# Kernel tuning notes

Measured on AMD Instinct MI355X. Metric: run time of the kernel, lower is better.

## Reference

```python
import jax, jax.numpy as jnp
import numpy as np

BITS = 4
N_PACK = 8          # 32-bit words / 4-bit values
GROUPSIZE = 128
MASK = (1 << BITS) - 1


def dequantize(qweight, qzeros, scales):
    """GPTQ/optimum-format int4 dequant.
    qweight: [in/8, out] int32, little-endian nibbles along packed (input) dim.
    qzeros:  [groups, out/8] int32, little-endian nibbles along packed (output) dim.
    scales:  [groups, out] float.
    Returns W: [in, out] float.
    """
    shifts = (jnp.arange(N_PACK, dtype=jnp.int32) * BITS)
    kpack, out_f = qweight.shape
    groups = scales.shape[0]
    # unpack weight nibbles -> [in, out]
    w_int = (qweight[:, None, :] >> shifts[None, :, None]) & MASK        # [in/8, 8, out]
    w_int = w_int.reshape(kpack * N_PACK, out_f)                          # [in, out]
    # unpack zero-point nibbles -> [groups, out]; optimum format adds 1 back
    zp = (qzeros[:, :, None] >> shifts[None, None, :]) & MASK             # [groups, out/8, 8]
    zp = zp.reshape(groups, out_f) + 1                                    # [groups, out]
    # group-wise dequant: (w - zp) * scale
    w_g = w_int.reshape(groups, GROUPSIZE, out_f).astype(scales.dtype)    # [G, gs, out]
    W = (w_g - zp[:, None, :].astype(scales.dtype)) * scales[:, None, :]
    return W.reshape(kpack * N_PACK, out_f)


def setup_inputs() -> dict:
    key = jax.random.key(0)
    k1, k2, k3, k4, k5 = jax.random.split(key, 5)
    in_f, out_f, groups = 4096, 11008, 4096 // GROUPSIZE
    tokens = 4096
    x = jax.random.normal(k1, (tokens, in_f), dtype=jnp.float32)
    qweight = jax.random.randint(k2, (in_f // N_PACK, out_f), 0, 2147483647, dtype=jnp.int32)
    qzeros = jax.random.randint(k3, (groups, out_f // N_PACK), 0, 2147483647, dtype=jnp.int32)
    scales = jax.random.uniform(k4, (groups, out_f), dtype=jnp.float32) * 0.01 + 0.001
    bias = jax.random.normal(k5, (out_f,), dtype=jnp.float32)
    return {"x": x, "qweight": qweight, "qzeros": qzeros, "scales": scales, "bias": bias}


def reference(x, qweight, qzeros, scales, bias):
    W = dequantize(qweight, qzeros, scales)   # [in, out]
    return x @ W + bias                        # F.linear(x, W.T, bias)
```

## Files before the change

### kernel.cpp

```cpp
#include <hip/hip_runtime.h>
#include <stdint.h>

typedef _Float16 h2 __attribute__((ext_vector_type(2)));
typedef _Float16 h8 __attribute__((ext_vector_type(8)));
typedef float f32x4 __attribute__((ext_vector_type(4)));

__device__ __forceinline__ uint32_t pk_cvt(float a, float b) {
  return __builtin_bit_cast(uint32_t, __builtin_amdgcn_cvt_pkrtz(a, b));
}

__device__ __forceinline__ uint32_t dq(uint32_t t, h2 z2, h2 s2) {
  h2 v = __builtin_bit_cast(h2, t);
  h2 w = (v - z2) * s2;
  return __builtin_bit_cast(uint32_t, w);
}

__device__ __forceinline__ uint32_t dq_lin(uint32_t u, h2 z2, h2 s2) {
  uint32_t t = (u & 0xFu) | ((u & 0xF0u) << 12) | 0x64006400u;
  return dq(t, z2, s2);
}

typedef __attribute__((address_space(1))) const uint32_t* gas_ptr;
typedef __attribute__((address_space(3))) uint32_t* las_ptr;
__device__ __forceinline__ void gll16(const _Float16* g, _Float16* l) {
  __builtin_amdgcn_global_load_lds((gas_ptr)g, (las_ptr)l, 16, 0, 0);
}

#define WAITVM(n) asm volatile("s_waitcnt vmcnt(" #n ")" ::: "memory")
#define WAITLGKM(n) asm volatile("s_waitcnt lgkmcnt(" #n ")" ::: "memory")
#define MEMFENCE  asm volatile("" ::: "memory")
#define SB __builtin_amdgcn_sched_barrier(0)

__global__ __launch_bounds__(256) void cvt_x_kernel(const float* __restrict__ x,
                                                    _Float16* __restrict__ xh,
                                                    size_t n) {
  size_t i = ((size_t)blockIdx.x * 256 + threadIdx.x) * 8;
  if (i >= n) return;
  float4 a = *(const float4*)(x + i);
  float4 b = *(const float4*)(x + i + 4);
  uint4 v = make_uint4(pk_cvt(a.x, a.y), pk_cvt(a.z, a.w),
                       pk_cvt(b.x, b.y), pk_cvt(b.z, b.w));
  *(uint4*)(xh + i) = v;
}

__global__ __launch_bounds__(512, 2) void gemm_f16_fusedB(
    const _Float16* __restrict__ A, const uint32_t* __restrict__ qweight,
    const uint32_t* __restrict__ qzeros, const float* __restrict__ scales,
    const float* __restrict__ bias, float* __restrict__ out,
    int M, int N, int K) {
  __shared__ _Float16 As[4][256 * 32];
  __shared__ _Float16 Bs[4][256 * 32];

  const int gx = gridDim.x, gy = gridDim.y;
  const int nwg = gx * gy;
  const int lin = blockIdx.y * gx + blockIdx.x;
  const int xcd = lin & 7, idx = lin >> 3;
  const int q8 = nwg >> 3, r8 = nwg & 7;
  const int wg = (xcd < r8 ? xcd * (q8 + 1) : r8 * (q8 + 1) + (xcd - r8) * q8) + idx;
  const int bn0 = (wg % gx) * 256;
  const int bm0 = (wg / gx) * 256;

  const int tid = threadIdx.x;
  const int lane = tid & 63;
  const int wave = tid >> 6;
  const int wm = wave >> 2;
  const int wn = wave & 3;

  f32x4 acc[8][4];
#pragma unroll
  for (int i = 0; i < 8; ++i)
#pragma unroll
    for (int j = 0; j < 4; ++j) acc[i][j] = (f32x4)0.f;

  const int srow = lane >> 2;
  const int sslot = (lane & 3) ^ ((lane >> 3) & 3);
  const _Float16* pSa0 = A + (size_t)(bm0 + 32 * wave + srow) * K + sslot * 8;
  const _Float16* pSa1 = pSa0 + (size_t)16 * K;
  const int dst_off = wave * 1024;

  const int bcol = tid & 255;
  const int kpo = tid >> 8;
  const int ncol = bn0 + bcol;
  const int NP = N >> 3;
  const uint32_t* qbase = qweight + ncol;
  const uint32_t* qzbase = qzeros + (ncol >> 3);
  const float* scbase = scales + ncol;
  const int bw0 = bcol * 32 + ((kpo)     ^ ((bcol >> 1) & 3)) * 8;
  const int bw1 = bcol * 32 + ((kpo + 2) ^ ((bcol >> 1) & 3)) * 8;

  const int fslot = ((lane >> 4) ^ ((lane >> 1) & 3)) * 8;
  const int aoff = (wm * 128 + (lane & 15)) * 32 + fslot;
  const int boff = (wn * 64 + (lane & 15)) * 32 + fslot;

  const int nt = K >> 5;

  uint32_t qE0 = 0, qE1 = 0, qzE = 0; float scE = 0.f;
  uint32_t qO0 = 0, qO1 = 0, qzO = 0; float scO = 0.f;

#define GLLA(u) {                                                         \
    const size_t ko_ = (size_t)(u) * 32;                                  \
    _Float16* da_ = &As[(u) & 3][0] + dst_off;                            \
    gll16(pSa0 + ko_, da_);                                               \
    gll16(pSa1 + ko_, da_ + 512);                                         \
  }

#define QLOAD(SET, u) {                                                   \
    const size_t kpb_ = (size_t)(u) * 4 + kpo;                            \
    q##SET##0 = qbase[kpb_ * N];                                          \
    q##SET##1 = qbase[(kpb_ + 2) * N];                                    \
    const int g_ = (u) >> 2;                                              \
    qz##SET = qzbase[(size_t)g_ * NP];                                    \
    sc##SET = scbase[(size_t)g_ * N];                                     \
  }

#define DEQW(SET, u) {                                                    \
    int zp_ = (qz##SET >> ((ncol & 7) * 4)) & 15;                         \
    _Float16 hz_ = (_Float16)(float)(1024 + zp_ + 1);                     \
    _Float16 hs_ = (_Float16)sc##SET;                                     \
    h2 z2_ = {hz_, hz_}, s2_ = {hs_, hs_};                                \
    _Float16* bb_ = &Bs[(u) & 3][0];                                      \
    uint4 v0_ = make_uint4(dq_lin(q##SET##0, z2_, s2_),                   \
                           dq_lin(q##SET##0 >> 8, z2_, s2_),              \
                           dq_lin(q##SET##0 >> 16, z2_, s2_),             \
                           dq_lin(q##SET##0 >> 24, z2_, s2_));            \
    uint4 v1_ = make_uint4(dq_lin(q##SET##1, z2_, s2_),                   \
                           dq_lin(q##SET##1 >> 8, z2_, s2_),              \
                           dq_lin(q##SET##1 >> 16, z2_, s2_),             \
                           dq_lin(q##SET##1 >> 24, z2_, s2_));            \
    *(uint4*)(bb_ + bw0) = v0_;                                           \
    *(uint4*)(bb_ + bw1) = v1_;                                           \
  }

#define ITER_BODY(T, CS, LS)                                              \
  {                                                                       \
    __builtin_amdgcn_s_barrier();                                         \
    MEMFENCE;                                                             \
    const int buf_ = (T) & 3;                                             \
    const _Float16* Ab_ = &As[buf_][0] + aoff;                            \
    const _Float16* Bb_ = &Bs[buf_][0] + boff;                            \
    h8 bf_[4], af0_[4], af1_[4];                                          \
    _Pragma("unroll") for (int r = 0; r < 4; ++r)                         \
        bf_[r] = *(const h8*)(Bb_ + r * 512);                             \
    _Pragma("unroll") for (int r = 0; r < 4; ++r)                         \
        af0_[r] = *(const h8*)(Ab_ + r * 512);                            \
    _Pragma("unroll") for (int r = 0; r < 4; ++r)                         \
        af1_[r] = *(const h8*)(Ab_ + (4 + r) * 512);                      \
    SB;                                                                   \
    if ((T) + 2 < nt) QLOAD(LS, (T) + 2);                                 \
    SB;                                                                   \
    if ((T) + 3 < nt) GLLA((T) + 3);                                      \
    SB;                                                                   \
    if ((T) + 1 < nt) {                                                   \
      if ((T) + 4 <= nt) { WAITVM(8); }                                   \
      else if ((T) + 3 == nt) { WAITVM(6); }                              \
      else { WAITVM(0); }                                                 \
      SB;                                                                 \
      DEQW(CS, (T) + 1);                                                  \
      WAITLGKM(6);                                                        \
    } else {                                                              \
      WAITLGKM(4);                                                        \
    }                                                                     \
    SB;                                                                   \
    __builtin_amdgcn_s_setprio(1);                                        \
    _Pragma("unroll") for (int r = 0; r < 4; ++r)                         \
      _Pragma("unroll") for (int j = 0; j < 4; ++j)                       \
        acc[r][j] = __builtin_amdgcn_mfma_f32_16x16x32_f16(               \
            af0_[r], bf_[j], acc[r][j], 0, 0, 0);                         \
    __builtin_amdgcn_s_setprio(0);                                        \
    WAITLGKM(0);                                                          \
    SB;                                                                   \
    __builtin_amdgcn_s_setprio(1);                                        \
    _Pragma("unroll") for (int r = 0; r < 4; ++r)                         \
      _Pragma("unroll") for (int j = 0; j < 4; ++j)                       \
        acc[4 + r][j] = __builtin_amdgcn_mfma_f32_16x16x32_f16(           \
            af1_[r], bf_[j], acc[4 + r][j], 0, 0, 0);                     \
    __builtin_amdgcn_s_setprio(0);                                        \
  }

  GLLA(0); SB;
  QLOAD(E, 0); SB;
  GLLA(1); SB;
  QLOAD(O, 1); SB;
  GLLA(2); SB;
  WAITVM(8);
  SB;
  DEQW(E, 0);
  WAITLGKM(0);

  for (int t = 0; t < nt; t += 2) {
    ITER_BODY(t, O, E);
    ITER_BODY(t + 1, E, O);
  }

  const int r0 = bm0 + wm * 128 + ((lane >> 4) << 2);
  const int c0 = bn0 + wn * 64 + (lane & 15);
#pragma unroll
  for (int j = 0; j < 4; ++j) {
    const int c = c0 + j * 16;
    const float bv = bias[c];
#pragma unroll
    for (int i = 0; i < 8; ++i) {
#pragma unroll
      for (int rr = 0; rr < 4; ++rr)
        out[(size_t)(r0 + i * 16 + rr) * N + c] = acc[i][j][rr] + bv;
    }
  }
#undef GLLA
#undef QLOAD
#undef DEQW
#undef ITER_BODY
}

#define LDK 40
__global__ __launch_bounds__(256) void gptq_gemm_fused(
    const float* __restrict__ x, const uint32_t* __restrict__ qweight,
    const uint32_t* __restrict__ qzeros, const float* __restrict__ scales,
    const float* __restrict__ bias, float* __restrict__ out,
    int M, int N, int K) {
  __shared__ _Float16 As[128 * LDK];
  __shared__ _Float16 Bs[128 * LDK];
  const int tid = threadIdx.x, lane = tid & 63, wave = tid >> 6;
  const int wm = wave & 1, wn = wave >> 1;
  const int bn0 = blockIdx.x * 128, bm0 = blockIdx.y * 128;
  const int sr = tid >> 1, sg0 = (tid & 1) * 2;
  const float* xrow = x + (size_t)(bm0 + sr) * K + sg0 * 8;
  const int colb = bn0 + sr;
  const int groups = K >> 7, NP = N >> 3;
  f32x4 acc[4][4];
#pragma unroll
  for (int i = 0; i < 4; ++i)
#pragma unroll
    for (int j = 0; j < 4; ++j) acc[i][j] = (f32x4)0.f;
  const _Float16* Ab = As + (wm * 64 + (lane & 15)) * LDK + (lane >> 4) * 8;
  const _Float16* Bb = Bs + (wn * 64 + (lane & 15)) * LDK + (lane >> 4) * 8;
  for (int g = 0; g < groups; ++g) {
    uint32_t qz = qzeros[(size_t)g * NP + (colb >> 3)];
    int zp = (qz >> ((colb & 7) * 4)) & 15;
    float sc = scales[(size_t)g * N + colb];
    _Float16 hz = (_Float16)(float)(1024 + zp + 1);
    _Float16 hs = (_Float16)sc;
    h2 z2 = {hz, hz}, s2 = {hs, hs};
#pragma unroll
    for (int kt = 0; kt < 4; ++kt) {
      const int k0 = g * 128 + kt * 32;
      const float* xr = xrow + k0;
      float4 fa0 = *(const float4*)(xr);
      float4 fa1 = *(const float4*)(xr + 4);
      float4 fa2 = *(const float4*)(xr + 8);
      float4 fa3 = *(const float4*)(xr + 12);
      const size_t kp = (size_t)(k0 >> 3) + sg0;
      uint32_t q0 = qweight[kp * N + colb];
      uint32_t q1 = qweight[(kp + 1) * N + colb];
      __syncthreads();
      uint4 av0 = make_uint4(pk_cvt(fa0.x, fa1.x), pk_cvt(fa0.y, fa1.y),
                             pk_cvt(fa0.z, fa1.z), pk_cvt(fa0.w, fa1.w));
      uint4 av1 = make_uint4(pk_cvt(fa2.x, fa3.x), pk_cvt(fa2.y, fa3.y),
                             pk_cvt(fa2.z, fa3.z), pk_cvt(fa2.w, fa3.w));
      *(uint4*)(As + sr * LDK + sg0 * 8) = av0;
      *(uint4*)(As + sr * LDK + sg0 * 8 + 8) = av1;
      uint4 bv0 = make_uint4(dq((q0 & 0x000F000Fu) | 0x64006400u, z2, s2),
                             dq(((q0 >> 4) & 0x000F000Fu) | 0x64006400u, z2, s2),
                             dq(((q0 >> 8) & 0x000F000Fu) | 0x64006400u, z2, s2),
                             dq(((q0 >> 12) & 0x000F000Fu) | 0x64006400u, z2, s2));
      uint4 bv1 = make_uint4(dq((q1 & 0x000F000Fu) | 0x64006400u, z2, s2),
                             dq(((q1 >> 4) & 0x000F000Fu) | 0x64006400u, z2, s2),
                             dq(((q1 >> 8) & 0x000F000Fu) | 0x64006400u, z2, s2),
                             dq(((q1 >> 12) & 0x000F000Fu) | 0x64006400u, z2, s2));
      *(uint4*)(Bs + sr * LDK + sg0 * 8) = bv0;
      *(uint4*)(Bs + sr * LDK + sg0 * 8 + 8) = bv1;
      __syncthreads();
      h8 af[4], bf[4];
#pragma unroll
      for (int i = 0; i < 4; ++i) {
        af[i] = *(const h8*)(Ab + i * 16 * LDK);
        bf[i] = *(const h8*)(Bb + i * 16 * LDK);
      }
#pragma unroll
      for (int i = 0; i < 4; ++i)
#pragma unroll
        for (int j = 0; j < 4; ++j)
          acc[i][j] = __builtin_amdgcn_mfma_f32_16x16x32_f16(af[i], bf[j],
                                                             acc[i][j], 0, 0, 0);
    }
  }
  const int r0 = bm0 + wm * 64 + (lane >> 4) * 4;
  const int c0 = bn0 + wn * 64 + (lane & 15);
#pragma unroll
  for (int j = 0; j < 4; ++j) {
    const int c = c0 + j * 16;
    const float bv = bias[c];
#pragma unroll
    for (int i = 0; i < 4; ++i)
#pragma unroll
      for (int rr = 0; rr < 4; ++rr)
        out[(size_t)(r0 + i * 16 + rr) * N + c] = acc[i][j][rr] + bv;
  }
}

extern "C" void kernel_launch(void* const* d_in, const int* in_sizes, int n_in,
                              void* d_out, int out_size, void* d_ws, size_t ws_size,
                              hipStream_t stream) {
  const float* x = (const float*)d_in[0];
  const uint32_t* qweight = (const uint32_t*)d_in[1];
  const uint32_t* qzeros = (const uint32_t*)d_in[2];
  const float* scales = (const float*)d_in[3];
  const float* bias = (const float*)d_in[4];
  float* out = (float*)d_out;

  const int out_f = in_sizes[4];
  const int groups = in_sizes[3] / out_f;
  const int in_f = groups * 128;
  const int tokens = in_sizes[0] / in_f;

  const size_t needA = (size_t)tokens * in_f * 2;
  const bool fits = (tokens % 256) == 0 && (out_f % 256) == 0 &&
                    (in_f % 64) == 0 && in_f >= 128;
  if (ws_size >= needA && fits) {
    _Float16* xh = (_Float16*)d_ws;
    size_t nx = (size_t)tokens * in_f;
    cvt_x_kernel<<<(nx + 2047) / 2048, 256, 0, stream>>>(x, xh, nx);

    dim3 gg(out_f / 256, tokens / 256);
    gemm_f16_fusedB<<<gg, 512, 0, stream>>>(xh, qweight, qzeros, scales, bias,
                                            out, tokens, out_f, in_f);
  } else {
    dim3 grid(out_f / 128, tokens / 128);
    gptq_gemm_fused<<<grid, 256, 0, stream>>>(x, qweight, qzeros, scales, bias,
                                              out, tokens, out_f, in_f);
  }
}
```

Before: 692.5 us.

## Cheapen int4 unpack via matched k-permutation and overlap dequant with MFMAs

The int4 unpack now extracts two nibbles per mask using one shift and one `& 0x000F000F`. This places weight nibbles (i, i+4) into each fp16 pair, so B's k-order is permuted within each group of 8. The x-to-fp16 conversion applies the same permutation to A, which keeps the dot product unchanged while cutting integer ALU work per dequant. The dequant-and-LDS-store step also moves between the two halves of the MFMA block, and several sched_barriers and lgkm waits are removed, so VALU work can hide under matrix ops. The risk is that the compiler's looser scheduling adds register pressure or misplaces waits around the shared buffers.

Result: faster. 646.6 us (-6.6%).

```diff
diff --git a/kernel.cpp b/kernel.cpp
--- a/kernel.cpp
+++ b/kernel.cpp
@@ -13,11 +13,6 @@
   h2 v = __builtin_bit_cast(h2, t);
   h2 w = (v - z2) * s2;
   return __builtin_bit_cast(uint32_t, w);
-}
-
-__device__ __forceinline__ uint32_t dq_lin(uint32_t u, h2 z2, h2 s2) {
-  uint32_t t = (u & 0xFu) | ((u & 0xF0u) << 12) | 0x64006400u;
-  return dq(t, z2, s2);
 }
 
 typedef __attribute__((address_space(1))) const uint32_t* gas_ptr;
@@ -38,8 +33,8 @@
   if (i >= n) return;
   float4 a = *(const float4*)(x + i);
   float4 b = *(const float4*)(x + i + 4);
-  uint4 v = make_uint4(pk_cvt(a.x, a.y), pk_cvt(a.z, a.w),
-                       pk_cvt(b.x, b.y), pk_cvt(b.z, b.w));
+  uint4 v = make_uint4(pk_cvt(a.x, b.x), pk_cvt(a.y, b.y),
+                       pk_cvt(a.z, b.z), pk_cvt(a.w, b.w));
   *(uint4*)(xh + i) = v;
 }
 
@@ -82,6 +77,7 @@
   const int kpo = tid >> 8;
   const int ncol = bn0 + bcol;
   const int NP = N >> 3;
+  const int zshift = (ncol & 7) * 4;
   const uint32_t* qbase = qweight + ncol;
   const uint32_t* qzbase = qzeros + (ncol >> 3);
   const float* scbase = scales + ncol;
@@ -114,19 +110,21 @@
   }
 
 #define DEQW(SET, u) {                                                    \
-    int zp_ = (qz##SET >> ((ncol & 7) * 4)) & 15;                         \
+    int zp_ = (qz##SET >> zshift) & 15;                                   \
     _Float16 hz_ = (_Float16)(float)(1024 + zp_ + 1);                     \
     _Float16 hs_ = (_Float16)sc##SET;                                     \
     h2 z2_ = {hz_, hz_}, s2_ = {hs_, hs_};                                \
     _Float16* bb_ = &Bs[(u) & 3][0];                                      \
-    uint4 v0_ = make_uint4(dq_lin(q##SET##0, z2_, s2_),                   \
-                           dq_lin(q##SET##0 >> 8, z2_, s2_),              \
-                           dq_lin(q##SET##0 >> 16, z2_, s2_),             \
-                           dq_lin(q##SET##0 >> 24, z2_, s2_));            \
-    uint4 v1_ = make_uint4(dq_lin(q##SET##1, z2_, s2_),                   \
-                           dq_lin(q##SET##1 >> 8, z2_, s2_),              \
-                           dq_lin(q##SET##1 >> 16, z2_, s2_),             \
-                           dq_lin(q##SET##1 >> 24, z2_, s2_));            \
+    uint4 v0_ = make_uint4(                                               \
+        dq((q##SET##0 & 0x000F000Fu) | 0x64006400u, z2_, s2_),            \
+        dq(((q##SET##0 >> 4) & 0x000F000Fu) | 0x64006400u, z2_, s2_),     \
+        dq(((q##SET##0 >> 8) & 0x000F000Fu) | 0x64006400u, z2_, s2_),     \
+        dq(((q##SET##0 >> 12) & 0x000F000Fu) | 0x64006400u, z2_, s2_));   \
+    uint4 v1_ = make_uint4(                                               \
+        dq((q##SET##1 & 0x000F000Fu) | 0x64006400u, z2_, s2_),            \
+        dq(((q##SET##1 >> 4) & 0x000F000Fu) | 0x64006400u, z2_, s2_),     \
+        dq(((q##SET##1 >> 8) & 0x000F000Fu) | 0x64006400u, z2_, s2_),     \
+        dq(((q##SET##1 >> 12) & 0x000F000Fu) | 0x64006400u, z2_, s2_));   \
     *(uint4*)(bb_ + bw0) = v0_;                                           \
     *(uint4*)(bb_ + bw1) = v1_;                                           \
   }
@@ -145,36 +143,25 @@
         af0_[r] = *(const h8*)(Ab_ + r * 512);                            \
     _Pragma("unroll") for (int r = 0; r < 4; ++r)                         \
         af1_[r] = *(const h8*)(Ab_ + (4 + r) * 512);                      \
-    SB;                                                                   \
     if ((T) + 2 < nt) QLOAD(LS, (T) + 2);                                 \
-    SB;                                                                   \
     if ((T) + 3 < nt) GLLA((T) + 3);                                      \
-    SB;                                                                   \
-    if ((T) + 1 < nt) {                                                   \
-      if ((T) + 4 <= nt) { WAITVM(8); }                                   \
-      else if ((T) + 3 == nt) { WAITVM(6); }                              \
-      else { WAITVM(0); }                                                 \
-      SB;                                                                 \
-      DEQW(CS, (T) + 1);                                                  \
-      WAITLGKM(6);                                                        \
-    } else {                                                              \
-      WAITLGKM(4);                                                        \
-    }                                                                     \
-    SB;                                                                   \
+    if ((T) + 4 <= nt) { WAITVM(8); }                                     \
+    else if ((T) + 3 == nt) { WAITVM(6); }                                \
+    else if ((T) + 2 == nt) { WAITVM(0); }                                \
+                                      \
     __builtin_amdgcn_s_setprio(1);                                        \
     _Pragma("unroll") for (int r = 0; r < 4; ++r)                         \
       _Pragma("unroll") for (int j = 0; j < 4; ++j)                       \
         acc[r][j] = __builtin_amdgcn_mfma_f32_16x16x32_f16(               \
             af0_[r], bf_[j], acc[r][j], 0, 0, 0);                         \
-    __builtin_amdgcn_s_setprio(0);                                        \
-    WAITLGKM(0);                                                          \
-    SB;                                                                   \
-    __builtin_amdgcn_s_setprio(1);                                        \
+    if ((T) + 1 < nt) DEQW(CS, (T) + 1);                                  \
     _Pragma("unroll") for (int r = 0; r < 4; ++r)                         \
       _Pragma("unroll") for (int j = 0; j < 4; ++j)                       \
         acc[4 + r][j] = __builtin_amdgcn_mfma_f32_16x16x32_f16(           \
             af1_[r], bf_[j], acc[4 + r][j], 0, 0, 0);                     \
     __builtin_amdgcn_s_setprio(0);                                        \
+    WAITLGKM(0);                                                          \
+    SB;                                                                   \
   }
 
   GLLA(0); SB;
```
